# Optimization experiments

Measured on AMD Instinct MI355X. Metric: run time of the kernel, lower is better.

Reference implementation:

```python
import jax, jax.numpy as jnp
import numpy as np

D_MODEL = 2048
DT_RANK = 64


def setup_inputs() -> dict:
    key = jax.random.key(0)
    ks = jax.random.split(key, 9)
    x = jax.random.normal(ks[0], (4, 2048, D_MODEL), dtype=jnp.float32)
    A = jax.random.normal(ks[1], (D_MODEL, D_MODEL), dtype=jnp.float32)
    B = jax.random.normal(ks[2], (D_MODEL, D_MODEL), dtype=jnp.float32)
    C = jax.random.normal(ks[3], (D_MODEL, D_MODEL), dtype=jnp.float32)
    Dp = jax.random.normal(ks[4], (1, D_MODEL), dtype=jnp.float32)
    # dt_project: Linear(d_model -> dt_rank); dt_project_out: Linear(dt_rank -> d_model)
    lim1 = 1.0 / np.sqrt(D_MODEL)
    W1 = jax.random.uniform(ks[5], (DT_RANK, D_MODEL), minval=-lim1, maxval=lim1, dtype=jnp.float32)
    b1 = jax.random.uniform(ks[6], (DT_RANK,), minval=-lim1, maxval=lim1, dtype=jnp.float32)
    lim2 = 1.0 / np.sqrt(DT_RANK)
    W2 = jax.random.uniform(ks[7], (D_MODEL, DT_RANK), minval=-lim2, maxval=lim2, dtype=jnp.float32)
    b2 = jax.random.uniform(ks[8], (D_MODEL,), minval=-lim2, maxval=lim2, dtype=jnp.float32)
    return {"x": x, "A": A, "B": B, "C": C, "Dp": Dp, "W1": W1, "b1": b1, "W2": W2, "b2": b2}


def reference(x, A, B, C, Dp, W1, b1, W2, b2):
    # dt = Linear_out(gelu(Linear_in(x)))  -- torch uses exact (erf) gelu
    h = jax.nn.gelu(jnp.einsum('bld,rd->blr', x, W1) + b1, approximate=False)
    dt = jnp.einsum('blr,dr->bld', h, W2) + b2
    # per-timestep loop collapses to one batched GEMM: x @ (A+B+C)
    out = jnp.einsum('bld,ds->bls', x, A + B + C)
    return out * dt + Dp  # Dp broadcasts (1, d_model)
```

## Files before the change

kernel.cpp:

```cpp
#include <hip/hip_runtime.h>
#include <stdint.h>

#define D 2048
#define R 64
#define M_TOTAL 8192

typedef float f32x4 __attribute__((ext_vector_type(4)));
typedef __bf16 bf16x8 __attribute__((ext_vector_type(8)));
typedef unsigned short u16x8 __attribute__((ext_vector_type(8)));
typedef unsigned short u16x4 __attribute__((ext_vector_type(4)));

__device__ __forceinline__ unsigned short f2bf(float f) {
  unsigned u = __builtin_bit_cast(unsigned, f);
  u += 0x7FFFu + ((u >> 16) & 1u);
  return (unsigned short)(u >> 16);
}

__device__ __forceinline__ u16x8 pack8(float4 a, float4 b) {
  u16x8 o = { f2bf(a.x), f2bf(a.y), f2bf(a.z), f2bf(a.w),
              f2bf(b.x), f2bf(b.y), f2bf(b.z), f2bf(b.w) };
  return o;
}

__device__ __forceinline__ void gload_lds16(const void* g, void* l) {
  __builtin_amdgcn_global_load_lds(
      (const __attribute__((address_space(1))) void*)g,
      (__attribute__((address_space(3))) void*)l, 16, 0, 0);
}

__device__ __forceinline__ void gload_lds_asm(const unsigned short* g, int lds_byte) {
  asm volatile("s_mov_b32 m0, %1\n\t"
               "global_load_lds_dwordx4 %0, off"
               :: "v"(g), "s"(lds_byte)
               : "memory");
}

__device__ __forceinline__ int lds_addr(const void* p) {
  return (int)(size_t)(const __attribute__((address_space(3))) void*)p;
}

__global__ __launch_bounds__(512) void prep_kernel(
    const float* __restrict__ x, const float* __restrict__ A,
    const float* __restrict__ B, const float* __restrict__ C,
    const float* __restrict__ w1, const float* __restrict__ b1,
    const float* __restrict__ w2,
    unsigned short* __restrict__ xbf, unsigned short* __restrict__ st,
    unsigned short* __restrict__ w2bf, unsigned short* __restrict__ hbf) {
  __shared__ unsigned short plds[24576];
  const int t = threadIdx.x;
  const int bx = blockIdx.x;

  if (bx < 256) {
    unsigned short* sX = plds;
    unsigned short* sW = plds + 8192;
    const int m0 = bx * 32;
    const int kq = t >> 7, u = t & 127;
    const int row = u >> 2, c = u & 3;
    const int row_w = u >> 1, cw0 = (u & 1) * 2;
    const float* xp = x + (size_t)(m0 + row) * D + kq * 512 + c * 8;
    const float* wp = w1 + (size_t)row_w * D + kq * 512 + cw0 * 8;
    unsigned short* xw = xbf + (size_t)(m0 + row) * D + kq * 512 + c * 8;
    unsigned short* sXw = sX + kq * 2048 + row * 32 + (c ^ ((row >> 1) & 3)) * 8;
    const int rw2 = (row_w >> 1) & 3;
    unsigned short* sWw0 = sW + kq * 4096 + row_w * 32 + (cw0 ^ rw2) * 8;
    unsigned short* sWw1 = sW + kq * 4096 + row_w * 32 + ((cw0 + 1) ^ rw2) * 8;
    const int w = t >> 6, l = t & 63, lm = l & 15, lk = l >> 4;
    const int kqw = w >> 1, rg = w & 1;
    const int rslot = (lk ^ ((lm >> 1) & 3)) * 8;
    const unsigned short* sXr = sX + kqw * 2048 + (rg * 16 + lm) * 32 + rslot;
    const unsigned short* sWr = sW + kqw * 4096 + lm * 32 + rslot;

    f32x4 acc[4] = {};
    float4 qx[2][2], qw[2][4];
#define HLOADX(P, KT) do { qx[P][0] = *(const float4*)(xp + (KT) * 32); \
                           qx[P][1] = *(const float4*)(xp + (KT) * 32 + 4); } while (0)
#define HLOADW(P, KT) do { qw[P][0] = *(const float4*)(wp + (KT) * 32); \
                           qw[P][1] = *(const float4*)(wp + (KT) * 32 + 4); \
                           qw[P][2] = *(const float4*)(wp + (KT) * 32 + 8); \
                           qw[P][3] = *(const float4*)(wp + (KT) * 32 + 12); } while (0)
    HLOADX(0, 0); HLOADW(0, 0); HLOADX(1, 1); HLOADW(1, 1);
#define HSTEP(P, KT) do { \
    u16x8 ox = pack8(qx[P][0], qx[P][1]); \
    *(u16x8*)(sXw + (P) * 1024) = ox; \
    *(u16x8*)(xw + (KT) * 32) = ox; \
    *(u16x8*)(sWw0 + (P) * 2048) = pack8(qw[P][0], qw[P][1]); \
    *(u16x8*)(sWw1 + (P) * 2048) = pack8(qw[P][2], qw[P][3]); \
    if ((KT) + 2 < 16) { HLOADX(P, (KT) + 2); HLOADW(P, (KT) + 2); } \
    __syncthreads(); \
    { bf16x8 a_ = __builtin_bit_cast(bf16x8, *(const u16x8*)(sXr + (P) * 1024)); \
      _Pragma("unroll") \
      for (int j = 0; j < 4; ++j) { \
        bf16x8 b_ = __builtin_bit_cast(bf16x8, *(const u16x8*)(sWr + (P) * 2048 + j * 512)); \
        acc[j] = __builtin_amdgcn_mfma_f32_16x16x32_bf16(a_, b_, acc[j], 0, 0, 0); \
      } } } while (0)
#pragma unroll 1
    for (int it = 0; it < 8; ++it) { HSTEP(0, it * 2); HSTEP(1, it * 2 + 1); }
#undef HSTEP
#undef HLOADX
#undef HLOADW

    __syncthreads();
    float* red = (float*)plds;
    if (kqw > 0) {
#pragma unroll
      for (int j = 0; j < 4; ++j)
        *(f32x4*)(red + (((((kqw - 1) * 2 + rg) * 4) + j) * 64 + l) * 4) = acc[j];
    }
    __syncthreads();
    if (kqw == 0) {
      int m_base = m0 + rg * 16 + lk * 4;
#pragma unroll
      for (int j = 0; j < 4; ++j) {
        f32x4 s = acc[j];
#pragma unroll
        for (int q = 1; q < 4; ++q)
          s += *(const f32x4*)(red + (((((q - 1) * 2 + rg) * 4) + j) * 64 + l) * 4);
        int n = j * 16 + lm;
        float bv = b1[n];
#pragma unroll
        for (int r = 0; r < 4; ++r) {
          float v = s[r] + bv;
          float g = 0.5f * v * (1.0f + erff(v * 0.70710678118654752f));
          hbf[(size_t)(m_base + r) * R + n] = f2bf(g);
        }
      }
    }
  } else if (bx < 768) {
    unsigned short (*lds)[68] = (unsigned short(*)[68])plds;
    const int id = bx - 256;
    const int k0 = (id >> 5) * 128, n0 = (id & 31) * 64;
#pragma unroll
    for (int q = 0; q < 4; ++q) {
      int rowq = q * 32 + (t >> 4);
      int col = (t & 15) * 4;
      size_t off = (size_t)(k0 + rowq) * D + n0 + col;
      float4 a = *(const float4*)(A + off);
      float4 b = *(const float4*)(B + off);
      float4 cc = *(const float4*)(C + off);
      u16x4 o = { f2bf(a.x + b.x + cc.x), f2bf(a.y + b.y + cc.y),
                  f2bf(a.z + b.z + cc.z), f2bf(a.w + b.w + cc.w) };
      *(u16x4*)(&lds[rowq][col]) = o;
    }
    __syncthreads();
    const int n = t >> 3, kc = (t & 7) * 16;
    u16x8 v0, v1;
#pragma unroll
    for (int jj = 0; jj < 8; ++jj) v0[jj] = lds[kc + jj][n];
#pragma unroll
    for (int jj = 0; jj < 8; ++jj) v1[jj] = lds[kc + 8 + jj][n];
    size_t ooff = (size_t)(n0 + n) * D + k0 + kc;
    *(u16x8*)(st + ooff) = v0;
    *(u16x8*)(st + ooff + 8) = v1;
  } else {
    const int NW4 = (D * R) / 4;
    for (int i = (bx - 768) * 512 + t; i < NW4; i += 4 * 512) {
      float4 v = ((const float4*)w2)[i];
      u16x4 o = { f2bf(v.x), f2bf(v.y), f2bf(v.z), f2bf(v.w) };
      *(u16x4*)(w2bf + (size_t)i * 4) = o;
    }
  }
}

__global__ __launch_bounds__(512, 2) void gemm_kernel(
    const unsigned short* __restrict__ xbf, const unsigned short* __restrict__ st,
    const unsigned short* __restrict__ hbf, const unsigned short* __restrict__ w2bf,
    const float* __restrict__ b2, const float* __restrict__ dp,
    float* __restrict__ out) {
  __shared__ unsigned short sA[2 * 16384];
  __shared__ unsigned short sB[2 * 16384];
  const int tid = threadIdx.x;
  const int w = tid >> 6, l = tid & 63, lk = l >> 4, lm = l & 15;
  const int wm = w >> 2, wn = w & 3;
  int bid = blockIdx.x;
  int wg = (bid & 7) * 32 + (bid >> 3);
  int mb = wg >> 3, nb = wg & 7;
  int m0 = mb * 256, n0 = nb * 256;

  const int kg = (tid & 7) ^ ((tid >> 3) & 7);
  const unsigned short* gA = xbf + (size_t)(m0 + (tid >> 3)) * D + kg * 8;
  const unsigned short* gB = st + (size_t)(n0 + (tid >> 3)) * D + kg * 8;
  const int sAb = __builtin_amdgcn_readfirstlane(lds_addr(sA) + w * 1024);
  const int sBb = __builtin_amdgcn_readfirstlane(lds_addr(sB) + w * 1024);

  const int s7 = lm & 7;
  const int gsw0 = (lk ^ s7) * 8;
  const int gsw1 = ((4 | lk) ^ s7) * 8;
  const int arow = (wm * 128 + lm) * 64;
  const int brow = (wn * 64 + lm) * 64;

  const int NT = D / 64;
  f32x4 acc[8][4] = {};
  bf16x8 aA[4][2], aB[4][2], bt[2][2], be[2][2], bo[2][2];

#define BUFA(S) (sA + (S) * 16384)
#define BUFB(S) (sB + (S) * 16384)
#define LD8(buf, off) __builtin_bit_cast(bf16x8, *(const u16x8*)((buf) + (off)))
#define SB0() __builtin_amdgcn_sched_barrier(0)
#define BAR() __builtin_amdgcn_s_barrier()
#define LGKM4() asm volatile("s_waitcnt lgkmcnt(4)" ::: "memory")
#define LGKM8() asm volatile("s_waitcnt lgkmcnt(8)" ::: "memory")

#define STAGE2(gptr, lbase, T, h, S) do { if ((T) < NT) { \
    const unsigned short* g_ = (gptr) + (size_t)((h) * 128) * D + (T) * 64; \
    int lb_ = (lbase) + (S) * 32768 + (h) * 16384; \
    gload_lds_asm(g_, lb_); \
    gload_lds_asm(g_ + 64 * D, lb_ + 8192); } } while (0)

#define RD_A03(S) do { _Pragma("unroll") for (int i = 0; i < 4; ++i) { \
    aA[i][0] = LD8(BUFA(S), arow + i * 1024 + gsw0); \
    aA[i][1] = LD8(BUFA(S), arow + i * 1024 + gsw1); } } while (0)
#define RD_A47(S) do { _Pragma("unroll") for (int i = 0; i < 4; ++i) { \
    aB[i][0] = LD8(BUFA(S), arow + (i + 4) * 1024 + gsw0); \
    aB[i][1] = LD8(BUFA(S), arow + (i + 4) * 1024 + gsw1); } } while (0)
#define RD_B23(S) do { _Pragma("unroll") for (int j = 0; j < 2; ++j) { \
    bt[j][0] = LD8(BUFB(S), brow + (j + 2) * 1024 + gsw0); \
    bt[j][1] = LD8(BUFB(S), brow + (j + 2) * 1024 + gsw1); } } while (0)
#define RD_B01(S, DST) do { _Pragma("unroll") for (int j = 0; j < 2; ++j) { \
    DST[j][0] = LD8(BUFB(S), brow + j * 1024 + gsw0); \
    DST[j][1] = LD8(BUFB(S), brow + j * 1024 + gsw1); } } while (0)

#define QUAD(AR, BR, IO, JO) do { \
    __builtin_amdgcn_s_setprio(1); \
    _Pragma("unroll") for (int i = 0; i < 4; ++i) \
    _Pragma("unroll") for (int j = 0; j < 2; ++j) { \
      acc[i + IO][j + JO] = __builtin_amdgcn_mfma_f32_16x16x32_bf16(AR[i][0], BR[j][0], acc[i + IO][j + JO], 0, 0, 0); \
      acc[i + IO][j + JO] = __builtin_amdgcn_mfma_f32_16x16x32_bf16(AR[i][1], BR[j][1], acc[i + IO][j + JO], 0, 0, 0); \
    } \
    __builtin_amdgcn_s_setprio(0); } while (0)

#define TILE(S, BCUR, BNXT, KT) do { \
     \
    RD_B23(S); \
    STAGE2(gB, sBb, (KT) + 2, 0, S); \
    SB0(); BAR(); LGKM4(); SB0(); \
    QUAD(aA, BCUR, 0, 0); \
    SB0(); BAR(); \
     \
    RD_A47(S); \
    STAGE2(gA, sAb, (KT) + 2, 0, S); \
    SB0(); BAR(); LGKM8(); SB0(); \
    QUAD(aA, bt, 0, 2); \
    if ((KT) < NT - 2) asm volatile("s_waitcnt vmcnt(4)" ::: "memory"); \
    else               asm volatile("s_waitcnt vmcnt(0)" ::: "memory"); \
    SB0(); BAR(); \
     \
    RD_A03((S) ^ 1); \
    STAGE2(gB, sBb, (KT) + 2, 1, S); \
    SB0(); BAR(); LGKM8(); SB0(); \
    QUAD(aB, bt, 4, 2); \
    SB0(); BAR(); \
     \
    RD_B01((S) ^ 1, BNXT); \
    STAGE2(gA, sAb, (KT) + 2, 1, S); \
    SB0(); BAR(); LGKM4(); SB0(); \
    QUAD(aB, BCUR, 4, 0); \
    SB0(); BAR(); } while (0)

  STAGE2(gB, sBb, 0, 0, 0); STAGE2(gA, sAb, 0, 0, 0);
  STAGE2(gB, sBb, 0, 1, 0); STAGE2(gA, sAb, 0, 1, 0);
  STAGE2(gB, sBb, 1, 0, 1); STAGE2(gA, sAb, 1, 0, 1);
  STAGE2(gB, sBb, 1, 1, 1); STAGE2(gA, sAb, 1, 1, 1);
  asm volatile("s_waitcnt vmcnt(8)" ::: "memory");
  BAR();
  RD_A03(0);
  RD_B01(0, be);
  SB0();

#pragma unroll 1
  for (int it = 0; it < NT / 2; ++it) {
    const int kt0 = it * 2;
    TILE(0, be, bo, kt0);
    TILE(1, bo, be, kt0 + 1);
  }

  bf16x8 wb0[4], wb1[4];
  float b2v[4], dpv[4];
#pragma unroll
  for (int j = 0; j < 4; ++j) {
    int n = n0 + wn * 64 + j * 16 + lm;
    const u16x8* wp = (const u16x8*)(w2bf + (size_t)n * R + lk * 8);
    wb0[j] = __builtin_bit_cast(bf16x8, wp[0]);
    wb1[j] = __builtin_bit_cast(bf16x8, wp[4]);
    b2v[j] = b2[n];
    dpv[j] = dp[n];
  }
#pragma unroll
  for (int mi = 0; mi < 8; ++mi) {
    int hrow = m0 + wm * 128 + mi * 16 + lm;
    const u16x8* hp = (const u16x8*)(hbf + (size_t)hrow * R + lk * 8);
    bf16x8 ha0 = __builtin_bit_cast(bf16x8, hp[0]);
    bf16x8 ha1 = __builtin_bit_cast(bf16x8, hp[4]);
    int mbase = m0 + wm * 128 + mi * 16 + lk * 4;
#pragma unroll
    for (int j = 0; j < 4; ++j) {
      f32x4 dt = {};
      dt = __builtin_amdgcn_mfma_f32_16x16x32_bf16(ha0, wb0[j], dt, 0, 0, 0);
      dt = __builtin_amdgcn_mfma_f32_16x16x32_bf16(ha1, wb1[j], dt, 0, 0, 0);
      int n = n0 + wn * 64 + j * 16 + lm;
#pragma unroll
      for (int r = 0; r < 4; ++r) {
        float val = acc[mi][j][r] * (dt[r] + b2v[j]) + dpv[j];
        out[(size_t)(mbase + r) * D + n] = val;
      }
    }
  }
#undef TILE
#undef QUAD
#undef RD_A03
#undef RD_A47
#undef RD_B23
#undef RD_B01
#undef STAGE2
#undef LGKM4
#undef LGKM8
#undef BAR
#undef SB0
#undef LD8
#undef BUFA
#undef BUFB
}

extern "C" void kernel_launch(void* const* d_in, const int* in_sizes, int n_in,
                              void* d_out, int out_size, void* d_ws, size_t ws_size,
                              hipStream_t stream) {
  const float* x  = (const float*)d_in[0];
  const float* A  = (const float*)d_in[1];
  const float* B  = (const float*)d_in[2];
  const float* C  = (const float*)d_in[3];
  const float* Dp = (const float*)d_in[4];
  const float* W1 = (const float*)d_in[5];
  const float* b1 = (const float*)d_in[6];
  const float* W2 = (const float*)d_in[7];
  const float* b2 = (const float*)d_in[8];
  float* out = (float*)d_out;

  uint8_t* ws = (uint8_t*)d_ws;
  unsigned short* xbf  = (unsigned short*)ws;
  unsigned short* st   = (unsigned short*)(ws + (32u << 20));
  unsigned short* w2bf = (unsigned short*)(ws + (40u << 20));
  unsigned short* hbf  = (unsigned short*)(ws + (41u << 20));

  prep_kernel<<<772, 512, 0, stream>>>(x, A, B, C, W1, b1, W2, xbf, st, w2bf, hbf);
  gemm_kernel<<<256, 512, 0, stream>>>(xbf, st, hbf, w2bf, b2, Dp, out);
}
```

Baseline: 98.41 us.

## Restructure GEMM mainloop into 4-stage K=32 pipeline with one barrier per step

The GEMM main loop moves from a 2-stage K=64 tile with four sub-phases and many barriers per tile to a 4-deep ring of K=32 LDS stages. Each step reads the next stage into alternating register sets, issues global-to-LDS loads three steps ahead, and runs all 32 MFMAs with a single barrier. The goal is less barrier and synchronisation overhead and deeper prefetch to hide global-load latency. The cost is twice as many loop iterations, smaller LDS tiles, and a different swizzle that may change bank-conflict behaviour.

```diff
diff --git a/kernel.cpp b/kernel.cpp
--- a/kernel.cpp
+++ b/kernel.cpp
@@ -166,8 +166,8 @@
     const unsigned short* __restrict__ hbf, const unsigned short* __restrict__ w2bf,
     const float* __restrict__ b2, const float* __restrict__ dp,
     float* __restrict__ out) {
-  __shared__ unsigned short sA[2 * 16384];
-  __shared__ unsigned short sB[2 * 16384];
+  __shared__ unsigned short sA[4 * 8192];
+  __shared__ unsigned short sB[4 * 8192];
   const int tid = threadIdx.x;
   const int w = tid >> 6, l = tid & 63, lk = l >> 4, lm = l & 15;
   const int wm = w >> 2, wn = w & 3;
@@ -176,101 +176,72 @@
   int mb = wg >> 3, nb = wg & 7;
   int m0 = mb * 256, n0 = nb * 256;
 
-  const int kg = (tid & 7) ^ ((tid >> 3) & 7);
-  const unsigned short* gA = xbf + (size_t)(m0 + (tid >> 3)) * D + kg * 8;
-  const unsigned short* gB = st + (size_t)(n0 + (tid >> 3)) * D + kg * 8;
+  const int kg = (tid & 3) ^ ((tid >> 2) & 3);
+  const unsigned short* gA = xbf + (size_t)(m0 + (tid >> 2)) * D + kg * 8;
+  const unsigned short* gB = st + (size_t)(n0 + (tid >> 2)) * D + kg * 8;
   const int sAb = __builtin_amdgcn_readfirstlane(lds_addr(sA) + w * 1024);
   const int sBb = __builtin_amdgcn_readfirstlane(lds_addr(sB) + w * 1024);
 
-  const int s7 = lm & 7;
-  const int gsw0 = (lk ^ s7) * 8;
-  const int gsw1 = ((4 | lk) ^ s7) * 8;
-  const int arow = (wm * 128 + lm) * 64;
-  const int brow = (wn * 64 + lm) * 64;
-
-  const int NT = D / 64;
+  const int gsw = (lk ^ (lm & 3)) * 8;
+  const int arow = (wm * 128 + lm) * 32;
+  const int brow = (wn * 64 + lm) * 32;
+
+  const int NT = D / 32;
   f32x4 acc[8][4] = {};
-  bf16x8 aA[4][2], aB[4][2], bt[2][2], be[2][2], bo[2][2];
-
-#define BUFA(S) (sA + (S) * 16384)
-#define BUFB(S) (sB + (S) * 16384)
+  bf16x8 aE[8], bE[4], aO[8], bO[4];
+
 #define LD8(buf, off) __builtin_bit_cast(bf16x8, *(const u16x8*)((buf) + (off)))
 #define SB0() __builtin_amdgcn_sched_barrier(0)
 #define BAR() __builtin_amdgcn_s_barrier()
-#define LGKM4() asm volatile("s_waitcnt lgkmcnt(4)" ::: "memory")
-#define LGKM8() asm volatile("s_waitcnt lgkmcnt(8)" ::: "memory")
-
-#define STAGE2(gptr, lbase, T, h, S) do { if ((T) < NT) { \
-    const unsigned short* g_ = (gptr) + (size_t)((h) * 128) * D + (T) * 64; \
-    int lb_ = (lbase) + (S) * 32768 + (h) * 16384; \
-    gload_lds_asm(g_, lb_); \
-    gload_lds_asm(g_ + 64 * D, lb_ + 8192); } } while (0)
-
-#define RD_A03(S) do { _Pragma("unroll") for (int i = 0; i < 4; ++i) { \
-    aA[i][0] = LD8(BUFA(S), arow + i * 1024 + gsw0); \
-    aA[i][1] = LD8(BUFA(S), arow + i * 1024 + gsw1); } } while (0)
-#define RD_A47(S) do { _Pragma("unroll") for (int i = 0; i < 4; ++i) { \
-    aB[i][0] = LD8(BUFA(S), arow + (i + 4) * 1024 + gsw0); \
-    aB[i][1] = LD8(BUFA(S), arow + (i + 4) * 1024 + gsw1); } } while (0)
-#define RD_B23(S) do { _Pragma("unroll") for (int j = 0; j < 2; ++j) { \
-    bt[j][0] = LD8(BUFB(S), brow + (j + 2) * 1024 + gsw0); \
-    bt[j][1] = LD8(BUFB(S), brow + (j + 2) * 1024 + gsw1); } } while (0)
-#define RD_B01(S, DST) do { _Pragma("unroll") for (int j = 0; j < 2; ++j) { \
-    DST[j][0] = LD8(BUFB(S), brow + j * 1024 + gsw0); \
-    DST[j][1] = LD8(BUFB(S), brow + j * 1024 + gsw1); } } while (0)
-
-#define QUAD(AR, BR, IO, JO) do { \
+
+#define STAGE_T(T) do { if ((T) < NT) { \
+    const unsigned short* ga_ = gA + (T) * 32; \
+    int la_ = sAb + ((T) & 3) * 16384; \
+    gload_lds_asm(ga_, la_); \
+    gload_lds_asm(ga_ + 128 * D, la_ + 8192); \
+    const unsigned short* gb_ = gB + (T) * 32; \
+    int lb_ = sBb + ((T) & 3) * 16384; \
+    gload_lds_asm(gb_, lb_); \
+    gload_lds_asm(gb_ + 128 * D, lb_ + 8192); } } while (0)
+
+#define RD_T(S, AR, BR) do { \
+    const unsigned short* bA_ = sA + (S) * 8192; \
+    const unsigned short* bB_ = sB + (S) * 8192; \
+    _Pragma("unroll") for (int i = 0; i < 8; ++i) \
+      AR[i] = LD8(bA_, arow + i * 512 + gsw); \
+    _Pragma("unroll") for (int j = 0; j < 4; ++j) \
+      BR[j] = LD8(bB_, brow + j * 512 + gsw); } while (0)
+
+#define MM32(AR, BR) do { \
     __builtin_amdgcn_s_setprio(1); \
-    _Pragma("unroll") for (int i = 0; i < 4; ++i) \
-    _Pragma("unroll") for (int j = 0; j < 2; ++j) { \
-      acc[i + IO][j + JO] = __builtin_amdgcn_mfma_f32_16x16x32_bf16(AR[i][0], BR[j][0], acc[i + IO][j + JO], 0, 0, 0); \
-      acc[i + IO][j + JO] = __builtin_amdgcn_mfma_f32_16x16x32_bf16(AR[i][1], BR[j][1], acc[i + IO][j + JO], 0, 0, 0); \
-    } \
+    _Pragma("unroll") for (int i = 0; i < 8; ++i) \
+    _Pragma("unroll") for (int j = 0; j < 4; ++j) \
+      acc[i][j] = __builtin_amdgcn_mfma_f32_16x16x32_bf16(AR[i], BR[j], acc[i][j], 0, 0, 0); \
     __builtin_amdgcn_s_setprio(0); } while (0)
 
-#define TILE(S, BCUR, BNXT, KT) do { \
-     \
-    RD_B23(S); \
-    STAGE2(gB, sBb, (KT) + 2, 0, S); \
-    SB0(); BAR(); LGKM4(); SB0(); \
-    QUAD(aA, BCUR, 0, 0); \
-    SB0(); BAR(); \
-     \
-    RD_A47(S); \
-    STAGE2(gA, sAb, (KT) + 2, 0, S); \
-    SB0(); BAR(); LGKM8(); SB0(); \
-    QUAD(aA, bt, 0, 2); \
-    if ((KT) < NT - 2) asm volatile("s_waitcnt vmcnt(4)" ::: "memory"); \
+#define PHASE(KT, CA, CB, NA, NB) do { \
+    RD_T(((KT) + 1) & 3, NA, NB); \
+    STAGE_T((KT) + 3); \
+    SB0(); \
+    asm volatile("s_waitcnt lgkmcnt(12)" ::: "memory"); \
+    SB0(); \
+    MM32(CA, CB); \
+    SB0(); \
+    if ((KT) < NT - 3) asm volatile("s_waitcnt vmcnt(4)" ::: "memory"); \
     else               asm volatile("s_waitcnt vmcnt(0)" ::: "memory"); \
-    SB0(); BAR(); \
-     \
-    RD_A03((S) ^ 1); \
-    STAGE2(gB, sBb, (KT) + 2, 1, S); \
-    SB0(); BAR(); LGKM8(); SB0(); \
-    QUAD(aB, bt, 4, 2); \
-    SB0(); BAR(); \
-     \
-    RD_B01((S) ^ 1, BNXT); \
-    STAGE2(gA, sAb, (KT) + 2, 1, S); \
-    SB0(); BAR(); LGKM4(); SB0(); \
-    QUAD(aB, BCUR, 4, 0); \
     SB0(); BAR(); } while (0)
 
-  STAGE2(gB, sBb, 0, 0, 0); STAGE2(gA, sAb, 0, 0, 0);
-  STAGE2(gB, sBb, 0, 1, 0); STAGE2(gA, sAb, 0, 1, 0);
-  STAGE2(gB, sBb, 1, 0, 1); STAGE2(gA, sAb, 1, 0, 1);
-  STAGE2(gB, sBb, 1, 1, 1); STAGE2(gA, sAb, 1, 1, 1);
-  asm volatile("s_waitcnt vmcnt(8)" ::: "memory");
+  STAGE_T(0); STAGE_T(1); STAGE_T(2);
+  asm volatile("s_waitcnt vmcnt(4)" ::: "memory");
   BAR();
-  RD_A03(0);
-  RD_B01(0, be);
+  RD_T(0, aE, bE);
   SB0();
 
 #pragma unroll 1
   for (int it = 0; it < NT / 2; ++it) {
     const int kt0 = it * 2;
-    TILE(0, be, bo, kt0);
-    TILE(1, bo, be, kt0 + 1);
+    PHASE(kt0, aE, bE, aO, bO);
+    PHASE(kt0 + 1, aO, bO, aE, bE);
   }
 
   bf16x8 wb0[4], wb1[4];
@@ -304,20 +275,13 @@
       }
     }
   }
-#undef TILE
-#undef QUAD
-#undef RD_A03
-#undef RD_A47
-#undef RD_B23
-#undef RD_B01
-#undef STAGE2
-#undef LGKM4
-#undef LGKM8
+#undef PHASE
+#undef MM32
+#undef RD_T
+#undef STAGE_T
 #undef BAR
 #undef SB0
 #undef LD8
-#undef BUFA
-#undef BUFB
 }
 
 extern "C" void kernel_launch(void* const* d_in, const int* in_sizes, int n_in,
```

New measurement: 102.1 us. 1.04x slower.
